# Kernel optimization log

Measured on AMD Instinct MI355X. Metric: run time of the kernel, lower is better.

The kernel has to match this reference:

```python
import jax, jax.numpy as jnp
import numpy as np

NB_HEADS = 12


def setup_inputs() -> dict:
    key = jax.random.key(0)
    ks = jax.random.split(key, 6)
    B, S, D, H = 4, 1024, 768, NB_HEADS
    x = jax.random.normal(ks[0], (B, S, D), dtype=jnp.float32)
    Wqkv = jax.random.normal(ks[1], (D, 3 * D), dtype=jnp.float32) * 0.02
    bqkv = jnp.zeros((3 * D,), dtype=jnp.float32)
    Wl = jax.random.normal(ks[2], (H, H), dtype=jnp.float32) * 0.3
    bl = jnp.zeros((H,), dtype=jnp.float32)
    Ww = jax.random.normal(ks[3], (H, H), dtype=jnp.float32) * 0.3
    bw = jnp.zeros((H,), dtype=jnp.float32)
    Wproj = jax.random.normal(ks[4], (D, D), dtype=jnp.float32) * 0.02
    bproj = jnp.zeros((D,), dtype=jnp.float32)
    return {"x": x, "Wqkv": Wqkv, "bqkv": bqkv, "Wl": Wl, "bl": bl,
            "Ww": Ww, "bw": bw, "Wproj": Wproj, "bproj": bproj}


def reference(x, Wqkv, bqkv, Wl, bl, Ww, bw, Wproj, bproj):
    B, S, D = x.shape
    H = NB_HEADS
    dh = D // H
    scale = dh ** (-0.5)
    # qkv projection: [B,S,3D] -> [3,B,H,S,dh]
    qkv = (x @ Wqkv + bqkv).reshape(B, S, 3, H, dh).transpose(2, 0, 3, 1, 4)
    q, k, v = qkv[0] * scale, qkv[1], qkv[2]
    # raw attention logits [B,H,S,S]
    attn = jnp.einsum('bhqd,bhkd->bhqk', q, k)
    # pre-softmax talking-heads mix across head dim (Dense over heads)
    attn = jnp.einsum('bhqk,hg->bgqk', attn, Wl) + bl[None, :, None, None]
    attn = jax.nn.softmax(attn, axis=-1)
    # post-softmax talking-heads mix
    attn = jnp.einsum('bhqk,hg->bgqk', attn, Ww) + bw[None, :, None, None]
    # attention-weighted values -> [B,S,D]
    out = jnp.einsum('bhqk,bhkd->bqhd', attn, v).reshape(B, S, D)
    return out @ Wproj + bproj
```

## Files before the change

### kernel.cpp

```cpp
#include <hip/hip_runtime.h>
#include <cstdint>

#define BB 4
#define SS 1024
#define DD 768
#define HH 12
#define DH 64

typedef unsigned short u16;
typedef unsigned int   u32;
typedef __attribute__((ext_vector_type(8))) short bf16x8;
typedef __attribute__((ext_vector_type(4))) float f32x4;

__device__ __forceinline__ u16 f2bf(float f) {
    u32 u = __float_as_uint(f);
    u += 0x7fffu + ((u >> 16) & 1u);
    return (u16)(u >> 16);
}
__device__ __forceinline__ float b2f(u32 lo16) {
    return __uint_as_float(lo16 << 16);
}

__device__ __forceinline__ float fast_exp2(float x) {
    return __builtin_amdgcn_exp2f(x);
}

#if __has_builtin(__builtin_amdgcn_cvt_pk_bf16_f32)
__device__ __forceinline__ u32 pack2(float a, float b) {
    auto r = __builtin_amdgcn_cvt_pk_bf16_f32(a, b);
    u32 v; __builtin_memcpy(&v, &r, 4); return v;
}
#else
__device__ __forceinline__ u32 pack2(float a, float b) {
    return (u32)f2bf(a) | ((u32)f2bf(b) << 16);
}
#endif

#define ASYNC16(gp, lp) __builtin_amdgcn_global_load_lds( \
    (const __attribute__((address_space(1))) void*)(gp),  \
    (__attribute__((address_space(3))) void*)(lp), 16, 0, 0)

template<int BM_, int BN_, class Epi>
__device__ __forceinline__ void mfma_gemm(
    const u16* __restrict__ A, const u16* __restrict__ B,
    int K, int lda, int ldb, int m0, int n0, const Epi& epi)
{
    constexpr int MI = BM_ / 32;
    constexpr int NJ = BN_ / 32;
    __shared__ u16 Alds[BM_ * 32];
    __shared__ u16 Blds[BN_ * 32];

    const int tid  = threadIdx.x;
    const int wave = tid >> 6;
    const int lane = tid & 63;
    const int wr = wave >> 1, wc = wave & 1;

    const int ar = lane >> 2;
    const int ac = (lane & 3) * 8;

    f32x4 acc[MI][NJ] = {};

    for (int k0 = 0; k0 < K; k0 += 32) {
        __syncthreads();
#pragma unroll
        for (int j = 0; j < BM_ / 64; ++j) {
            const int rb = wave * (BM_ / 4) + j * 16;
            ASYNC16(A + (size_t)(m0 + rb + ar) * lda + k0 + ac, &Alds[rb * 32]);
        }
#pragma unroll
        for (int j = 0; j < BN_ / 64; ++j) {
            const int rb = wave * (BN_ / 4) + j * 16;
            ASYNC16(B + (size_t)(n0 + rb + ar) * ldb + k0 + ac, &Blds[rb * 32]);
        }
        __syncthreads();

        bf16x8 af[MI], bfr[NJ];
#pragma unroll
        for (int mi = 0; mi < MI; ++mi)
            af[mi] = *(const bf16x8*)&Alds[(wr * (BM_ / 2) + mi * 16 + (lane & 15)) * 32 + (lane >> 4) * 8];
#pragma unroll
        for (int nj = 0; nj < NJ; ++nj)
            bfr[nj] = *(const bf16x8*)&Blds[(wc * (BN_ / 2) + nj * 16 + (lane & 15)) * 32 + (lane >> 4) * 8];
#pragma unroll
        for (int mi = 0; mi < MI; ++mi)
#pragma unroll
            for (int nj = 0; nj < NJ; ++nj)
                acc[mi][nj] = __builtin_amdgcn_mfma_f32_16x16x32_bf16(
                    af[mi], bfr[nj], acc[mi][nj], 0, 0, 0);
    }

#pragma unroll
    for (int mi = 0; mi < MI; ++mi)
#pragma unroll
        for (int nj = 0; nj < NJ; ++nj)
#pragma unroll
            for (int r = 0; r < 4; ++r)
                epi(m0 + wr * (BM_ / 2) + mi * 16 + (lane >> 4) * 4 + r,
                    n0 + wc * (BN_ / 2) + nj * 16 + (lane & 15),
                    acc[mi][nj][r]);
}

#define CPAD 136

__global__ __launch_bounds__(256) void qkv_gemm_kernel(
    const u16* __restrict__ xb, const u16* __restrict__ Wt,
    const float* __restrict__ bias,
    u16* __restrict__ qb, u16* __restrict__ kb, u16* __restrict__ vb)
{
    __shared__ u16 Alds[128 * 32];
    __shared__ u16 Blds[128 * 32];
    __shared__ u16 Clds[128 * CPAD];

    const int tid  = threadIdx.x;
    const int wave = tid >> 6;
    const int lane = tid & 63;
    const int wr = wave >> 1, wc = wave & 1;
    const int ar = lane >> 2;
    const int ac = (lane & 3) * 8;
    const int m0 = blockIdx.y * 128, n0 = blockIdx.x * 128;

    f32x4 acc[4][4] = {};

    for (int k0 = 0; k0 < DD; k0 += 32) {
        __syncthreads();
#pragma unroll
        for (int j = 0; j < 2; ++j) {
            const int rb = wave * 32 + j * 16;
            ASYNC16(xb + (size_t)(m0 + rb + ar) * DD + k0 + ac, &Alds[rb * 32]);
            ASYNC16(Wt + (size_t)(n0 + rb + ar) * DD + k0 + ac, &Blds[rb * 32]);
        }
        __syncthreads();

        bf16x8 af[4], bfr[4];
#pragma unroll
        for (int mi = 0; mi < 4; ++mi)
            af[mi] = *(const bf16x8*)&Alds[(wr * 64 + mi * 16 + (lane & 15)) * 32 + (lane >> 4) * 8];
#pragma unroll
        for (int nj = 0; nj < 4; ++nj)
            bfr[nj] = *(const bf16x8*)&Blds[(wc * 64 + nj * 16 + (lane & 15)) * 32 + (lane >> 4) * 8];
#pragma unroll
        for (int mi = 0; mi < 4; ++mi)
#pragma unroll
            for (int nj = 0; nj < 4; ++nj)
                acc[mi][nj] = __builtin_amdgcn_mfma_f32_16x16x32_bf16(
                    af[mi], bfr[nj], acc[mi][nj], 0, 0, 0);
    }

    const int c  = n0 / DD;
    const int w0 = n0 - c * DD;
    const int hA = w0 >> 6;
    const float qs = (c == 0) ? 0.125f : 1.0f;
#pragma unroll
    for (int mi = 0; mi < 4; ++mi)
#pragma unroll
        for (int nj = 0; nj < 4; ++nj)
#pragma unroll
            for (int r = 0; r < 4; ++r) {
                const int row = wr * 64 + mi * 16 + (lane >> 4) * 4 + r;
                const int col = wc * 64 + nj * 16 + (lane & 15);
                Clds[row * CPAD + col] = f2bf((acc[mi][nj][r] + bias[n0 + col]) * qs);
            }
    __syncthreads();

    u16* const dst = (c == 0) ? qb : (c == 1) ? kb : vb;
    const int b = m0 >> 10;
#pragma unroll
    for (int j = 0; j < 8; ++j) {
        const int idx = j * 256 + tid;
        const int row = idx >> 4, u4 = idx & 15;
        const int half = u4 >> 3, d8 = u4 & 7;
        const int h = hA + half;
        const int s = (m0 + row) & 1023;
        const uint4 v = *(const uint4*)&Clds[row * CPAD + half * 64 + d8 * 8];
        *(uint4*)&dst[(((size_t)(b * HH + h) << 10) + s) * DH + d8 * 8] = v;
    }
}

__global__ __launch_bounds__(256) void vtrans_kernel(
    const u16* __restrict__ vb, u16* __restrict__ vt)
{
    __shared__ u16 t[64 * 72];
    const int tid = threadIdx.x;
    const int bh = blockIdx.y;
    const int s0 = blockIdx.x * 64;
    const u16* src = vb + ((size_t)bh << 16) + (size_t)s0 * DH;

#pragma unroll
    for (int j = 0; j < 2; ++j) {
        const int idx = j * 256 + tid;
        const int row = idx >> 3, u4 = idx & 7;
        *(uint4*)&t[row * 72 + u4 * 8] = *(const uint4*)&src[row * DH + u4 * 8];
    }
    __syncthreads();

#pragma unroll
    for (int j = 0; j < 2; ++j) {
        const int idx = j * 256 + tid;
        const int d = idx >> 3, u4 = idx & 7;
        u16 tmp[8];
#pragma unroll
        for (int i = 0; i < 8; ++i) tmp[i] = t[(u4 * 8 + i) * 72 + d];
        *(uint4*)&vt[((size_t)bh * DH + d) * SS + s0 + u4 * 8] = *(const uint4*)tmp;
    }
}

__global__ __launch_bounds__(256) void qk_gemm_kernel(
    const u16* __restrict__ qb, const u16* __restrict__ kb,
    u16* __restrict__ attn, int bh0)
{
    __shared__ u16 Alds[128 * 32];
    __shared__ u16 Blds[128 * 32];
    __shared__ u16 Clds[128 * CPAD];

    const int tid  = threadIdx.x;
    const int wave = tid >> 6;
    const int lane = tid & 63;
    const int wr = wave >> 1, wc = wave & 1;
    const int ar = lane >> 2;
    const int ac = (lane & 3) * 8;
    const int m0 = blockIdx.y * 128, n0 = blockIdx.x * 128;

    const int bhL = blockIdx.z;
    const u16* A = qb + (size_t)(bh0 + bhL) * SS * DH;
    const u16* B = kb + (size_t)(bh0 + bhL) * SS * DH;
    u16* C = attn + (size_t)bhL * SS * SS;

    f32x4 acc[4][4] = {};

#pragma unroll
    for (int k0 = 0; k0 < DH; k0 += 32) {
        __syncthreads();
#pragma unroll
        for (int j = 0; j < 2; ++j) {
            const int rb = wave * 32 + j * 16;
            ASYNC16(A + (size_t)(m0 + rb + ar) * DH + k0 + ac, &Alds[rb * 32]);
            ASYNC16(B + (size_t)(n0 + rb + ar) * DH + k0 + ac, &Blds[rb * 32]);
        }
        __syncthreads();

        bf16x8 af[4], bfr[4];
#pragma unroll
        for (int mi = 0; mi < 4; ++mi)
            af[mi] = *(const bf16x8*)&Alds[(wr * 64 + mi * 16 + (lane & 15)) * 32 + (lane >> 4) * 8];
#pragma unroll
        for (int nj = 0; nj < 4; ++nj)
            bfr[nj] = *(const bf16x8*)&Blds[(wc * 64 + nj * 16 + (lane & 15)) * 32 + (lane >> 4) * 8];
#pragma unroll
        for (int mi = 0; mi < 4; ++mi)
#pragma unroll
            for (int nj = 0; nj < 4; ++nj)
                acc[mi][nj] = __builtin_amdgcn_mfma_f32_16x16x32_bf16(
                    af[mi], bfr[nj], acc[mi][nj], 0, 0, 0);
    }

#pragma unroll
    for (int mi = 0; mi < 4; ++mi)
#pragma unroll
        for (int nj = 0; nj < 4; ++nj)
#pragma unroll
            for (int r = 0; r < 4; ++r) {
                const int row = wr * 64 + mi * 16 + (lane >> 4) * 4 + r;
                const int col = wc * 64 + nj * 16 + (lane & 15);
                Clds[row * CPAD + col] = f2bf(acc[mi][nj][r]);
            }
    __syncthreads();

#pragma unroll
    for (int j = 0; j < 8; ++j) {
        const int idx = j * 256 + tid;
        const int row = idx >> 4, u4 = idx & 15;
        *(uint4*)&C[(size_t)(m0 + row) * SS + n0 + u4 * 8] =
            *(const uint4*)&Clds[row * CPAD + u4 * 8];
    }
}

__global__ __launch_bounds__(256) void pv_gemm_kernel(
    const u16* __restrict__ attn2, const u16* __restrict__ vt,
    u16* __restrict__ ctx, int bh0)
{
    const int bhL = blockIdx.z;
    const int bh = bh0 + bhL;
    const int b = bh / HH, h = bh % HH;
    const u16* A = attn2 + (size_t)bhL * SS * SS;
    const u16* B = vt + (size_t)bh * DH * SS;
    u16* C = ctx + (size_t)b * SS * DD + h * DH;
    struct Epi {
        u16* C;
        __device__ void operator()(int m, int n, float v) const {
            C[(size_t)m * DD + n] = f2bf(v);
        }
    } epi{C};
    mfma_gemm<64, 64>(A, B, SS, SS, SS, blockIdx.y * 64, 0, epi);
}

__global__ __launch_bounds__(256) void proj_gemm_kernel(
    const u16* __restrict__ ctx, const u16* __restrict__ Wt,
    const float* __restrict__ bias, float* __restrict__ out)
{
    struct Epi {
        float* out; const float* bias;
        __device__ void operator()(int m, int n, float v) const {
            out[(size_t)m * DD + n] = v + bias[n];
        }
    } epi{out, bias};
    mfma_gemm<128, 64>(ctx, Wt, DD, DD, DD, blockIdx.y * 128, blockIdx.x * 64, epi);
}

#define BSTRIDE 1028

__global__ __launch_bounds__(256) void mix_softmax_kernel(
    const u16* __restrict__ attn, u16* __restrict__ attn2,
    const float* __restrict__ Wl, const float* __restrict__ bl,
    const float* __restrict__ Ww, const float* __restrict__ bw)
{
    __shared__ u16 buf[HH * BSTRIDE];
    __shared__ float wsum[4][16];
    __shared__ float invd[16];

    const int tid  = threadIdx.x;
    const int wave = tid >> 6;
    const int lane = tid & 63;
    const int u    = lane >> 4;
    const int ln   = lane & 15;
    const int bL = blockIdx.x >> 10;
    const int qi = blockIdx.x & (SS - 1);
    const size_t gbase = ((size_t)bL * HH * SS + qi) * SS + tid * 4;
    const int kc = tid * 4;

#pragma unroll
    for (int h = 0; h < HH; ++h)
        *(uint2*)&buf[h * BSTRIDE + kc] = *(const uint2*)&attn[gbase + (size_t)h * SS * SS];

    bf16x8 a1;
    {
        u16 t[8];
#pragma unroll
        for (int j = 0; j < 8; ++j) {
            const int k = u * 8 + j;
            t[j] = (k < HH && ln < HH) ? f2bf(Wl[k * HH + ln] * 1.44269504f) : (u16)0;
        }
        __builtin_memcpy(&a1, t, 16);
    }
    f32x4 c1 = {0.f, 0.f, 0.f, 0.f};
#pragma unroll
    for (int r = 0; r < 4; ++r) {
        const int g = u * 4 + r;
        c1[r] = (g < HH) ? bl[g] * 1.44269504f : 0.f;
    }

    __syncthreads();

    const int posbase = wave * 256;

    u32 plo[16], phi[16];
    float part[4] = {0.f, 0.f, 0.f, 0.f};

#pragma unroll
    for (int mi = 0; mi < 16; ++mi) {
        const int pos = posbase + mi * 16 + ln;
        u16 t[8];
#pragma unroll
        for (int j = 0; j < 8; ++j) {
            const int k = u * 8 + j;
            t[j] = (k < HH) ? buf[k * BSTRIDE + pos] : (u16)0;
        }
        bf16x8 bfrag; __builtin_memcpy(&bfrag, t, 16);
        f32x4 d = __builtin_amdgcn_mfma_f32_16x16x32_bf16(a1, bfrag, c1, 0, 0, 0);
        const float e0 = fast_exp2(d[0]);
        const float e1 = fast_exp2(d[1]);
        const float e2 = fast_exp2(d[2]);
        const float e3 = fast_exp2(d[3]);
        part[0] += e0; part[1] += e1; part[2] += e2; part[3] += e3;
        plo[mi] = pack2(e0, e1);
        phi[mi] = pack2(e2, e3);
    }

#pragma unroll
    for (int off = 1; off < 16; off <<= 1) {
#pragma unroll
        for (int r = 0; r < 4; ++r) part[r] += __shfl_xor(part[r], off);
    }
    if (ln == 0) {
#pragma unroll
        for (int r = 0; r < 4; ++r) wsum[wave][u * 4 + r] = part[r];
    }
    __syncthreads();
    if (tid < 16)
        invd[tid] = 1.f / (wsum[0][tid] + wsum[1][tid] + wsum[2][tid] + wsum[3][tid]);
    __syncthreads();

    bf16x8 a2;
    {
        u16 t[8];
#pragma unroll
        for (int j = 0; j < 8; ++j) {
            const int k = u * 8 + j;
            t[j] = (k < HH && ln < HH) ? f2bf(Ww[k * HH + ln] * invd[k]) : (u16)0;
        }
        __builtin_memcpy(&a2, t, 16);
    }
    f32x4 c2 = {0.f, 0.f, 0.f, 0.f};
#pragma unroll
    for (int r = 0; r < 4; ++r) {
        const int g = u * 4 + r;
        c2[r] = (g < HH) ? bw[g] : 0.f;
    }

    const int srcA = ln + ((u == 1) ? 32 : 16);
#pragma unroll
    for (int mi = 0; mi < 16; ++mi) {
        const u32 wlo = plo[mi], whi = phi[mi];
        const u32 slo = (u32)__shfl((int)wlo, srcA);
        const u32 shi = (u32)__shfl((int)whi, srcA);
        u32 wv[4];
        wv[0] = (u == 0) ? wlo : ((u == 1) ? slo : 0u);
        wv[1] = (u == 0) ? whi : ((u == 1) ? shi : 0u);
        wv[2] = (u == 0) ? slo : 0u;
        wv[3] = (u == 0) ? shi : 0u;
        bf16x8 b2; __builtin_memcpy(&b2, wv, 16);
        f32x4 d = __builtin_amdgcn_mfma_f32_16x16x32_bf16(a2, b2, c2, 0, 0, 0);

        const int pos = posbase + mi * 16 + ln;
        const u32 p01 = pack2(d[0], d[1]);
        const u32 p23 = pack2(d[2], d[3]);
        if (u < 3) {
            buf[(u * 4 + 0) * BSTRIDE + pos] = (u16)p01;
            buf[(u * 4 + 1) * BSTRIDE + pos] = (u16)(p01 >> 16);
            buf[(u * 4 + 2) * BSTRIDE + pos] = (u16)p23;
            buf[(u * 4 + 3) * BSTRIDE + pos] = (u16)(p23 >> 16);
        }
    }
    __syncthreads();

#pragma unroll
    for (int g = 0; g < HH; ++g)
        *(uint2*)&attn2[gbase + (size_t)g * SS * SS] =
            *(const uint2*)&buf[g * BSTRIDE + kc];
}


__global__ __launch_bounds__(256) void cvt_bf16_kernel(
    const float* __restrict__ in, u16* __restrict__ out, int n8)
{
    const int i = blockIdx.x * 256 + threadIdx.x;
    if (i >= n8) return;
    const float4 a = ((const float4*)in)[i * 2];
    const float4 b = ((const float4*)in)[i * 2 + 1];
    uint4 p;
    p.x = pack2(a.x, a.y); p.y = pack2(a.z, a.w);
    p.z = pack2(b.x, b.y); p.w = pack2(b.z, b.w);
    ((uint4*)out)[i] = p;
}

__global__ __launch_bounds__(256) void cvt_transpose_kernel(
    const float* __restrict__ in, u16* __restrict__ out, int R, int C)
{
    __shared__ float t[32][33];
    const int c0 = blockIdx.x * 32, r0 = blockIdx.y * 32;
    const int tr = threadIdx.x >> 3;
    const int tc = (threadIdx.x & 7) * 4;
    const float4 v = *(const float4*)&in[(size_t)(r0 + tr) * C + c0 + tc];
    t[tc + 0][tr] = v.x; t[tc + 1][tr] = v.y;
    t[tc + 2][tr] = v.z; t[tc + 3][tr] = v.w;
    __syncthreads();
    uint2 p;
    p.x = pack2(t[tr][tc + 0], t[tr][tc + 1]);
    p.y = pack2(t[tr][tc + 2], t[tr][tc + 3]);
    *(uint2*)&out[(size_t)(c0 + tr) * R + r0 + tc] = p;
}

extern "C" void kernel_launch(void* const* d_in, const int* in_sizes, int n_in,
                              void* d_out, int out_size, void* d_ws, size_t ws_size,
                              hipStream_t stream)
{
    const float* x     = (const float*)d_in[0];
    const float* Wqkv  = (const float*)d_in[1];
    const float* bqkv  = (const float*)d_in[2];
    const float* Wl    = (const float*)d_in[3];
    const float* bl    = (const float*)d_in[4];
    const float* Ww    = (const float*)d_in[5];
    const float* bw    = (const float*)d_in[6];
    const float* Wproj = (const float*)d_in[7];
    const float* bproj = (const float*)d_in[8];
    float* out = (float*)d_out;

    const size_t N_XB  = (size_t)BB * SS * DD;
    const size_t N_QB  = (size_t)BB * HH * SS * DH;
    const size_t N_WT  = (size_t)DD * 3 * DD;
    const size_t N_WP  = (size_t)DD * DD;
    const size_t N_AT1 = (size_t)HH * SS * SS;

    u16* xb  = (u16*)d_ws;
    u16* qb  = xb  + N_XB;
    u16* kb  = qb  + N_QB;
    u16* vb  = kb  + N_QB;
    u16* vt  = vb  + N_QB;
    u16* ctx = vt  + N_QB;
    u16* Wqkv_t = ctx + N_XB;
    u16* Wproj_t = Wqkv_t + N_WT;
    u16* attn = Wproj_t + N_WP;

    const size_t fixed_bytes = (size_t)(N_XB * 2 + N_QB * 4 + N_WT + N_WP) * 2;
    int b_per = BB;
    while (b_per > 1 &&
           fixed_bytes + (size_t)b_per * N_AT1 * 2 * 2 > ws_size)
        b_per >>= 1;
    const int n_iter = BB / b_per;
    u16* attn2 = attn + (size_t)b_per * N_AT1;

    const dim3 blk(256);

    cvt_bf16_kernel<<<dim3((N_XB / 8 + 255) / 256), blk, 0, stream>>>(x, xb, (int)(N_XB / 8));
    cvt_transpose_kernel<<<dim3(3 * DD / 32, DD / 32), blk, 0, stream>>>(Wqkv, Wqkv_t, DD, 3 * DD);
    cvt_transpose_kernel<<<dim3(DD / 32, DD / 32), blk, 0, stream>>>(Wproj, Wproj_t, DD, DD);

    qkv_gemm_kernel<<<dim3(3 * DD / 128, BB * SS / 128), blk, 0, stream>>>(
        xb, Wqkv_t, bqkv, qb, kb, vb);
    vtrans_kernel<<<dim3(SS / 64, BB * HH), blk, 0, stream>>>(vb, vt);

    for (int it = 0; it < n_iter; ++it) {
        const int bh0 = it * b_per * HH;
        qk_gemm_kernel<<<dim3(SS / 128, SS / 128, b_per * HH), blk, 0, stream>>>(
            qb, kb, attn, bh0);
        mix_softmax_kernel<<<dim3(b_per * SS), blk, 0, stream>>>(
            attn, attn2, Wl, bl, Ww, bw);
        pv_gemm_kernel<<<dim3(1, SS / 64, b_per * HH), blk, 0, stream>>>(
            attn2, vt, ctx, bh0);
    }

    proj_gemm_kernel<<<dim3(DD / 64, BB * SS / 128), blk, 0, stream>>>(
        ctx, Wproj_t, bproj, out);
}
```

Before: 255.9 us.

## Store mix-softmax LDS tile key-major so MFMA fragments load as vectors

The shared buffer in the talking-heads mix/softmax kernel changes from head-major (12 rows of 1028) to key-major (1024 rows of 24 halves). Each thread transposes its loaded values in registers with byte-perm ops, so MFMA B fragments become single 16-byte LDS reads instead of eight scalar u16 gathers. The intermediate exp values are written back to LDS and re-read for the second MFMA, replacing the register arrays and cross-lane shuffles. This removes scalar LDS traffic and register pressure, at the cost of extra LDS round trips, possible bank conflicts from the 48-byte row stride, and perm work on both load and store.

```diff
diff --git a/kernel.cpp b/kernel.cpp
--- a/kernel.cpp
+++ b/kernel.cpp
@@ -306,14 +306,14 @@
     mfma_gemm<128, 64>(ctx, Wt, DD, DD, DD, blockIdx.y * 128, blockIdx.x * 64, epi);
 }
 
-#define BSTRIDE 1028
+#define ROWB 24
 
 __global__ __launch_bounds__(256) void mix_softmax_kernel(
     const u16* __restrict__ attn, u16* __restrict__ attn2,
     const float* __restrict__ Wl, const float* __restrict__ bl,
     const float* __restrict__ Ww, const float* __restrict__ bw)
 {
-    __shared__ u16 buf[HH * BSTRIDE];
+    __shared__ u16 buf[SS * ROWB];
     __shared__ float wsum[4][16];
     __shared__ float invd[16];
 
@@ -327,9 +327,28 @@
     const size_t gbase = ((size_t)bL * HH * SS + qi) * SS + tid * 4;
     const int kc = tid * 4;
 
-#pragma unroll
-    for (int h = 0; h < HH; ++h)
-        *(uint2*)&buf[h * BSTRIDE + kc] = *(const uint2*)&attn[gbase + (size_t)h * SS * SS];
+    {
+        uint2 src[HH];
+#pragma unroll
+        for (int h = 0; h < HH; ++h)
+            src[h] = *(const uint2*)&attn[gbase + (size_t)h * SS * SS];
+
+#pragma unroll
+        for (int i = 0; i < 4; ++i) {
+            const u32 sel = (i & 1) ? 0x07060302u : 0x05040100u;
+            u32 w[6];
+#pragma unroll
+            for (int j = 0; j < 6; ++j) {
+                const u32 lo = (i < 2) ? src[2 * j].x     : src[2 * j].y;
+                const u32 hi = (i < 2) ? src[2 * j + 1].x : src[2 * j + 1].y;
+                w[j] = __builtin_amdgcn_perm(hi, lo, sel);
+            }
+            uint4 q0; q0.x = w[0]; q0.y = w[1]; q0.z = w[2]; q0.w = w[3];
+            uint4 q1; q1.x = w[4]; q1.y = w[5]; q1.z = 0u;   q1.w = 0u;
+            *(uint4*)&buf[(kc + i) * ROWB + 0] = q0;
+            *(uint4*)&buf[(kc + i) * ROWB + 8] = q1;
+        }
+    }
 
     bf16x8 a1;
     {
@@ -351,28 +370,24 @@
     __syncthreads();
 
     const int posbase = wave * 256;
-
-    u32 plo[16], phi[16];
+    const int fragoff = (u & 1) * 8;
+
     float part[4] = {0.f, 0.f, 0.f, 0.f};
-
 #pragma unroll
     for (int mi = 0; mi < 16; ++mi) {
         const int pos = posbase + mi * 16 + ln;
-        u16 t[8];
-#pragma unroll
-        for (int j = 0; j < 8; ++j) {
-            const int k = u * 8 + j;
-            t[j] = (k < HH) ? buf[k * BSTRIDE + pos] : (u16)0;
-        }
-        bf16x8 bfrag; __builtin_memcpy(&bfrag, t, 16);
-        f32x4 d = __builtin_amdgcn_mfma_f32_16x16x32_bf16(a1, bfrag, c1, 0, 0, 0);
+        const bf16x8 bfrag = *(const bf16x8*)&buf[pos * ROWB + fragoff];
+        const f32x4 d = __builtin_amdgcn_mfma_f32_16x16x32_bf16(a1, bfrag, c1, 0, 0, 0);
         const float e0 = fast_exp2(d[0]);
         const float e1 = fast_exp2(d[1]);
         const float e2 = fast_exp2(d[2]);
         const float e3 = fast_exp2(d[3]);
         part[0] += e0; part[1] += e1; part[2] += e2; part[3] += e3;
-        plo[mi] = pack2(e0, e1);
-        phi[mi] = pack2(e2, e3);
+        if (u < 3) {
+            uint2 p;
+            p.x = pack2(e0, e1); p.y = pack2(e2, e3);
+            *(uint2*)&buf[pos * ROWB + u * 4] = p;
+        }
     }
 
 #pragma unroll
@@ -386,7 +401,7 @@
     }
     __syncthreads();
     if (tid < 16)
-        invd[tid] = 1.f / (wsum[0][tid] + wsum[1][tid] + wsum[2][tid] + wsum[3][tid]);
+        invd[tid] = 1.0f / (wsum[0][tid] + wsum[1][tid] + wsum[2][tid] + wsum[3][tid]);
     __syncthreads();
 
     bf16x8 a2;
@@ -406,36 +421,37 @@
         c2[r] = (g < HH) ? bw[g] : 0.f;
     }
 
-    const int srcA = ln + ((u == 1) ? 32 : 16);
 #pragma unroll
     for (int mi = 0; mi < 16; ++mi) {
-        const u32 wlo = plo[mi], whi = phi[mi];
-        const u32 slo = (u32)__shfl((int)wlo, srcA);
-        const u32 shi = (u32)__shfl((int)whi, srcA);
-        u32 wv[4];
-        wv[0] = (u == 0) ? wlo : ((u == 1) ? slo : 0u);
-        wv[1] = (u == 0) ? whi : ((u == 1) ? shi : 0u);
-        wv[2] = (u == 0) ? slo : 0u;
-        wv[3] = (u == 0) ? shi : 0u;
-        bf16x8 b2; __builtin_memcpy(&b2, wv, 16);
-        f32x4 d = __builtin_amdgcn_mfma_f32_16x16x32_bf16(a2, b2, c2, 0, 0, 0);
-
         const int pos = posbase + mi * 16 + ln;
-        const u32 p01 = pack2(d[0], d[1]);
-        const u32 p23 = pack2(d[2], d[3]);
+        const bf16x8 bfrag = *(const bf16x8*)&buf[pos * ROWB + fragoff];
+        const f32x4 d = __builtin_amdgcn_mfma_f32_16x16x32_bf16(a2, bfrag, c2, 0, 0, 0);
         if (u < 3) {
-            buf[(u * 4 + 0) * BSTRIDE + pos] = (u16)p01;
-            buf[(u * 4 + 1) * BSTRIDE + pos] = (u16)(p01 >> 16);
-            buf[(u * 4 + 2) * BSTRIDE + pos] = (u16)p23;
-            buf[(u * 4 + 3) * BSTRIDE + pos] = (u16)(p23 >> 16);
-        }
-    }
-    __syncthreads();
-
-#pragma unroll
-    for (int g = 0; g < HH; ++g)
-        *(uint2*)&attn2[gbase + (size_t)g * SS * SS] =
-            *(const uint2*)&buf[g * BSTRIDE + kc];
+            uint2 p;
+            p.x = pack2(d[0], d[1]); p.y = pack2(d[2], d[3]);
+            *(uint2*)&buf[pos * ROWB + u * 4] = p;
+        }
+    }
+    __syncthreads();
+
+    {
+        u32 rw[4][6];
+#pragma unroll
+        for (int i = 0; i < 4; ++i) {
+            const uint4 a = *(const uint4*)&buf[(kc + i) * ROWB + 0];
+            const uint2 b = *(const uint2*)&buf[(kc + i) * ROWB + 8];
+            rw[i][0] = a.x; rw[i][1] = a.y; rw[i][2] = a.z;
+            rw[i][3] = a.w; rw[i][4] = b.x; rw[i][5] = b.y;
+        }
+#pragma unroll
+        for (int g = 0; g < HH; ++g) {
+            const u32 sel = (g & 1) ? 0x07060302u : 0x05040100u;
+            uint2 p;
+            p.x = __builtin_amdgcn_perm(rw[1][g >> 1], rw[0][g >> 1], sel);
+            p.y = __builtin_amdgcn_perm(rw[3][g >> 1], rw[2][g >> 1], sel);
+            *(uint2*)&attn2[gbase + (size_t)g * SS * SS] = p;
+        }
+    }
 }
 
 
```

After: 248.2 us. 1.03x faster.
